# Kernel tuning notes

Measured on AMD Instinct MI355X. Metric: run time of the kernel, lower is better.

Reference implementation:

```python
import jax, jax.numpy as jnp
import numpy as np

B, C, O, K, H, W, CH = 32, 256, 256, 3, 56, 56, 4  # batch, in_planes, out_planes, kernel, spatial, in_chunk
STRIDE, PAD, DIL = 1, 1, 1


def setup_inputs() -> dict:
    key = jax.random.key(0)
    ks = jax.random.split(key, 5)
    gain = np.sqrt(2.0).astype(np.float32)  # calculate_gain('relu')
    x = jax.random.normal(ks[0], (B, C, H, W), jnp.float32)
    # CWFF: fc1 1x1 conv (C->C, no bias), fc2 1x1 conv (C->CH*C, bias)
    fc1_w = jax.random.normal(ks[1], (C, C), jnp.float32) * np.sqrt(2.0 / C).astype(np.float32)  # kaiming fan_out
    fc2_w = jax.random.normal(ks[2], (CH * C, C), jnp.float32) * np.sqrt(2.0 / (CH * C)).astype(np.float32)
    fc2_b = jnp.zeros((CH * C,), jnp.float32)
    cog_weight = jax.random.normal(ks[3], (O, CH, K, K), jnp.float32) * (gain * (CH * K * K) ** -0.5)
    weight = jax.random.normal(ks[4], (O, C, K, K), jnp.float32) * (gain * (C * K * K) ** -0.5)
    return dict(x=x, fc1_w=fc1_w, fc2_w=fc2_w, fc2_b=fc2_b, cog_weight=cog_weight, weight=weight)


def reference(x, fc1_w, fc2_w, fc2_b, cog_weight, weight):
    # CWFF: global avg pool -> 1x1 conv -> relu -> 1x1 conv
    pooled = x.mean(axis=(2, 3))                       # [B, C]
    h = jax.nn.relu(pooled @ fc1_w.T)                  # [B, C]
    kern = h @ fc2_w.T + fc2_b                         # [B, CH*C]
    # torch view(-1, in_chunk, 1, 1): channel dim splits as (c, ch)
    kern = kern.reshape(B, C, CH)                      # [B, C, CH]
    # cognitive weights: conv2d(cog_weight, kernel) == contraction over in_chunk
    cw = jnp.einsum('bct,otij->bocij', kern, cog_weight)   # [B, O, C, K, K]
    dyn_w = jax.nn.sigmoid(cw) * weight[None]               # per-sample kernels [B, O, C, K, K]
    # per-sample conv (groups=B in the original grouped-conv trick)
    def conv1(xi, wi):
        return jax.lax.conv_general_dilated(
            xi[None], wi,
            window_strides=(STRIDE, STRIDE),
            padding=[(PAD, PAD), (PAD, PAD)],
            rhs_dilation=(DIL, DIL))[0]
    return jax.vmap(conv1)(x, dyn_w)                   # [B, O, H, W]
```

## Files before the change

kernel.cpp:

```cpp
#include <hip/hip_runtime.h>

typedef unsigned short u16;
typedef __attribute__((ext_vector_type(4))) float f32x4;
typedef __attribute__((ext_vector_type(8))) short s16x8;
typedef __attribute__((ext_vector_type(4))) unsigned short u16x4;

static __device__ __forceinline__ u16 f2bf(float f) {
    unsigned int x = __float_as_uint(f);
    x += 0x7fffu + ((x >> 16) & 1u);
    return (u16)(x >> 16);
}

__global__ __launch_bounds__(256) void pool_kernel(const float* __restrict__ x,
                                                   float* __restrict__ pooled) {
    int bc = blockIdx.x;
    const float* p = x + (size_t)bc * 3136;
    float s = 0.f;
    for (int i = threadIdx.x; i < 784; i += 256) {
        f32x4 v = *(const f32x4*)(p + i * 4);
        s += v.x + v.y + v.z + v.w;
    }
#pragma unroll
    for (int off = 32; off; off >>= 1) s += __shfl_xor(s, off);
    __shared__ float red[4];
    int lane = threadIdx.x & 63, wave = threadIdx.x >> 6;
    if (lane == 0) red[wave] = s;
    __syncthreads();
    if (threadIdx.x == 0)
        pooled[bc] = (red[0] + red[1] + red[2] + red[3]) * (1.0f / 3136.0f);
}

__global__ __launch_bounds__(256) void fc1_kernel(const float* __restrict__ pooled,
                                                  const float* __restrict__ w,
                                                  float* __restrict__ h) {
    __shared__ float pv[256];
    int b = blockIdx.x >> 6;
    pv[threadIdx.x] = pooled[b * 256 + threadIdx.x];
    __syncthreads();
    int lane = threadIdx.x & 63, wave = threadIdx.x >> 6;
    int i = ((blockIdx.x & 63) << 2) + wave;
    f32x4 v = *(const f32x4*)(w + i * 256 + lane * 4);
    float s = v.x * pv[lane * 4 + 0] + v.y * pv[lane * 4 + 1] +
              v.z * pv[lane * 4 + 2] + v.w * pv[lane * 4 + 3];
#pragma unroll
    for (int off = 32; off; off >>= 1) s += __shfl_xor(s, off);
    if (lane == 0) h[b * 256 + i] = fmaxf(s, 0.f);
}

__global__ __launch_bounds__(256) void fc2_kernel(const float* __restrict__ h,
                                                  const float* __restrict__ w,
                                                  const float* __restrict__ bias,
                                                  float* __restrict__ kern) {
    __shared__ float hv[256];
    int b = blockIdx.x >> 8;
    hv[threadIdx.x] = h[b * 256 + threadIdx.x];
    __syncthreads();
    int lane = threadIdx.x & 63, wave = threadIdx.x >> 6;
    int i = ((blockIdx.x & 255) << 2) + wave;
    f32x4 v = *(const f32x4*)(w + i * 256 + lane * 4);
    float s = v.x * hv[lane * 4 + 0] + v.y * hv[lane * 4 + 1] +
              v.z * hv[lane * 4 + 2] + v.w * hv[lane * 4 + 3];
#pragma unroll
    for (int off = 32; off; off >>= 1) s += __shfl_xor(s, off);
    if (lane == 0) kern[b * 1024 + i] = s + bias[i];
}

__global__ __launch_bounds__(256) void dynw_kernel(const float* __restrict__ kern,
                                                   const float* __restrict__ cogw,
                                                   const float* __restrict__ wgt,
                                                   u16* __restrict__ dynw) {
    __shared__ float wl[2304];
    const int o = blockIdx.x & 255;
    const int bg = blockIdx.x >> 8;
    const int c = threadIdx.x;
    const float* wo = wgt + (size_t)o * 2304;
#pragma unroll
    for (int j = 0; j < 9; ++j)
        wl[j * 256 + c] = wo[j * 256 + c];
    __syncthreads();

    float cg0[9], cg1[9], cg2[9], cg3[9];
#pragma unroll
    for (int p = 0; p < 9; ++p) {
        cg0[p] = cogw[(o * 4 + 0) * 9 + p];
        cg1[p] = cogw[(o * 4 + 1) * 9 + p];
        cg2[p] = cogw[(o * 4 + 2) * 9 + p];
        cg3[p] = cogw[(o * 4 + 3) * 9 + p];
    }
    float w9[9];
#pragma unroll
    for (int p = 0; p < 9; ++p) w9[p] = wl[c * 9 + p];

    for (int b = bg * 8; b < bg * 8 + 8; ++b) {
        f32x4 k4 = *(const f32x4*)(kern + b * 1024 + c * 4);
        u16* dst = dynw + (size_t)(b * 256 + o) * 9 * 256 + c;
#pragma unroll
        for (int p = 0; p < 9; ++p) {
            float cw = k4.x * cg0[p] + k4.y * cg1[p] + k4.z * cg2[p] + k4.w * cg3[p];
            float sg = 1.0f / (1.0f + __expf(-cw));
            dst[p * 256] = f2bf(sg * w9[p]);
        }
    }
}

#define LDSW 40
__global__ __launch_bounds__(256, 2) void conv_kernel(const float* __restrict__ x,
                                                      const u16* __restrict__ dynw,
                                                      float* __restrict__ out) {
    __shared__ u16 lds[4 * 58 * LDSW];
    const int tid = threadIdx.x;
    const int wave = tid >> 6, lane = tid & 63;
    const int l15 = lane & 15, quad = lane >> 4;
    const int gid = blockIdx.x;
    const int slot = gid >> 3;
    const int b = (gid & 7) * 4 + slot / 28;
    const int stile = slot % 28;
    const int y0 = stile * 2;

    if (tid < 64) {
        int side = tid & 1, yy = (tid >> 1) & 3, cg = tid >> 3;
        *(u16x4*)&lds[(yy * 58 + (side ? 57 : 0)) * LDSW + cg * 4] = (u16x4){0, 0, 0, 0};
    }

    f32x4 acc[4][7];
#pragma unroll
    for (int mf = 0; mf < 4; ++mf)
#pragma unroll
        for (int nf = 0; nf < 7; ++nf) acc[mf][nf] = (f32x4){0.f, 0.f, 0.f, 0.f};

    int bbase[7];
#pragma unroll
    for (int nf = 0; nf < 7; ++nf) {
        int n = nf * 16 + l15;
        int r = (n >= 56) ? 1 : 0;
        int xx = n - 56 * r;
        bbase[nf] = (r * 58 + xx) * LDSW + quad * 8;
    }
    const u16* Abase = dynw + ((size_t)b * 256 + wave * 64 + l15) * 2304 + quad * 8;
    const float* Xb = x + (size_t)b * 256 * 3136;

    __syncthreads();
    for (int cc = 0; cc < 8; ++cc) {
#pragma unroll
        for (int it = 0; it < 7; ++it) {
            int i = it * 256 + tid;
            int q = i / 56;
            int xx = i - q * 56;
            int yy = q & 3;
            int cg = q >> 2;
            int yg = y0 - 1 + yy;
            u16x4 w = (u16x4){0, 0, 0, 0};
            if ((unsigned)yg < 56u) {
                const float* src = Xb + (size_t)(cc * 32 + cg * 4) * 3136 + yg * 56 + xx;
                w.x = f2bf(src[0]);
                w.y = f2bf(src[3136]);
                w.z = f2bf(src[2 * 3136]);
                w.w = f2bf(src[3 * 3136]);
            }
            *(u16x4*)&lds[(yy * 58 + 1 + xx) * LDSW + cg * 4] = w;
        }
        __syncthreads();
#pragma unroll
        for (int p = 0; p < 9; ++p) {
            const int dy = p / 3, dx = p % 3;
            const int tapoff = (dy * 58 + dx) * LDSW;
            s16x8 a0 = *(const s16x8*)(Abase + 0 * 36864 + p * 256 + cc * 32);
            s16x8 a1 = *(const s16x8*)(Abase + 1 * 36864 + p * 256 + cc * 32);
            s16x8 a2 = *(const s16x8*)(Abase + 2 * 36864 + p * 256 + cc * 32);
            s16x8 a3 = *(const s16x8*)(Abase + 3 * 36864 + p * 256 + cc * 32);
#pragma unroll
            for (int nf = 0; nf < 7; ++nf) {
                s16x8 bf = *(const s16x8*)(&lds[bbase[nf] + tapoff]);
                acc[0][nf] = __builtin_amdgcn_mfma_f32_16x16x32_bf16(a0, bf, acc[0][nf], 0, 0, 0);
                acc[1][nf] = __builtin_amdgcn_mfma_f32_16x16x32_bf16(a1, bf, acc[1][nf], 0, 0, 0);
                acc[2][nf] = __builtin_amdgcn_mfma_f32_16x16x32_bf16(a2, bf, acc[2][nf], 0, 0, 0);
                acc[3][nf] = __builtin_amdgcn_mfma_f32_16x16x32_bf16(a3, bf, acc[3][nf], 0, 0, 0);
            }
        }
        __syncthreads();
    }
#pragma unroll
    for (int mf = 0; mf < 4; ++mf) {
        int o = wave * 64 + mf * 16 + quad * 4;
        size_t obase = ((size_t)b * 256 + o) * 3136 + (size_t)stile * 112 + l15;
#pragma unroll
        for (int nf = 0; nf < 7; ++nf) {
#pragma unroll
            for (int r = 0; r < 4; ++r)
                out[obase + (size_t)r * 3136 + nf * 16] = acc[mf][nf][r];
        }
    }
}

extern "C" void kernel_launch(void* const* d_in, const int* in_sizes, int n_in,
                              void* d_out, int out_size, void* d_ws, size_t ws_size,
                              hipStream_t stream) {
    const float* x    = (const float*)d_in[0];
    const float* fc1w = (const float*)d_in[1];
    const float* fc2w = (const float*)d_in[2];
    const float* fc2b = (const float*)d_in[3];
    const float* cogw = (const float*)d_in[4];
    const float* wgt  = (const float*)d_in[5];
    float* out = (float*)d_out;

    char* ws = (char*)d_ws;
    float* pooled = (float*)ws;
    float* h      = (float*)(ws + 32768);
    float* kern   = (float*)(ws + 65536);
    u16*   dynw   = (u16*)(ws + 196608);

    pool_kernel<<<8192, 256, 0, stream>>>(x, pooled);
    fc1_kernel<<<2048, 256, 0, stream>>>(pooled, fc1w, h);
    fc2_kernel<<<8192, 256, 0, stream>>>(h, fc2w, fc2b, kern);
    dynw_kernel<<<1024, 256, 0, stream>>>(kern, cogw, wgt, dynw);
    conv_kernel<<<896, 256, 0, stream>>>(x, dynw, out);
}
```

Before: 384.6 us.

## Double-buffer conv input tiles in LDS with register prefetch of next chunk

The conv kernel now keeps two LDS buffers for the input halo tile. It issues global loads for the next 32-channel chunk into registers before running the MFMA loop on the current chunk, then converts those values to bf16 and writes them into the other buffer. This lets global-load latency overlap with matrix compute and removes one barrier per iteration. In exchange it uses 28 extra float registers plus precomputed offsets, which raises register pressure under the 2-blocks-per-SM launch bound, and it doubles LDS use.

```diff
diff --git a/kernel.cpp b/kernel.cpp
--- a/kernel.cpp
+++ b/kernel.cpp
@@ -107,7 +107,7 @@
 __global__ __launch_bounds__(256, 2) void conv_kernel(const float* __restrict__ x,
                                                       const u16* __restrict__ dynw,
                                                       float* __restrict__ out) {
-    __shared__ u16 lds[4 * 58 * LDSW];
+    __shared__ u16 lds[2][4 * 58 * LDSW];
     const int tid = threadIdx.x;
     const int wave = tid >> 6, lane = tid & 63;
     const int l15 = lane & 15, quad = lane >> 4;
@@ -117,9 +117,10 @@
     const int stile = slot % 28;
     const int y0 = stile * 2;
 
-    if (tid < 64) {
-        int side = tid & 1, yy = (tid >> 1) & 3, cg = tid >> 3;
-        *(u16x4*)&lds[(yy * 58 + (side ? 57 : 0)) * LDSW + cg * 4] = (u16x4){0, 0, 0, 0};
+    if (tid < 128) {
+        int cg = tid & 7, yy = (tid >> 3) & 3, side = (tid >> 5) & 1, bu = tid >> 6;
+        *(u16x4*)&lds[bu][(yy * 58 + (side ? 57 : 0)) * LDSW + cg * 4] =
+            (u16x4){0, 0, 0, 0};
     }
 
     f32x4 acc[4][7];
@@ -139,27 +140,44 @@
     const u16* Abase = dynw + ((size_t)b * 256 + wave * 64 + l15) * 2304 + quad * 8;
     const float* Xb = x + (size_t)b * 256 * 3136;
 
-    __syncthreads();
+    int st_goff[7], st_lds[7];
+    bool st_ok[7];
+#pragma unroll
+    for (int it = 0; it < 7; ++it) {
+        int i = it * 256 + tid;
+        int q = i / 56;
+        int xx = i - q * 56;
+        int yy = q & 3, cg = q >> 2;
+        int yg = y0 - 1 + yy;
+        st_ok[it] = (unsigned)yg < 56u;
+        st_goff[it] = cg * 4 * 3136 + (st_ok[it] ? yg * 56 + xx : 0);
+        st_lds[it] = (yy * 58 + 1 + xx) * LDSW + cg * 4;
+    }
+
+    float p0[7], p1[7], p2[7], p3[7];
+#define LOADC(cc)                                                         \
+    _Pragma("unroll") for (int it = 0; it < 7; ++it) {                    \
+        const float* s = Xb + (size_t)(cc) * 32 * 3136 + st_goff[it];     \
+        p0[it] = st_ok[it] ? s[0] : 0.f;                                  \
+        p1[it] = st_ok[it] ? s[3136] : 0.f;                               \
+        p2[it] = st_ok[it] ? s[2 * 3136] : 0.f;                           \
+        p3[it] = st_ok[it] ? s[3 * 3136] : 0.f;                           \
+    }
+#define WRITEC(bu)                                                        \
+    _Pragma("unroll") for (int it = 0; it < 7; ++it) {                    \
+        u16x4 w = (u16x4){f2bf(p0[it]), f2bf(p1[it]),                     \
+                          f2bf(p2[it]), f2bf(p3[it])};                    \
+        *(u16x4*)&lds[bu][st_lds[it]] = w;                                \
+    }
+
+    LOADC(0)
+    WRITEC(0)
+    __syncthreads();
+
     for (int cc = 0; cc < 8; ++cc) {
-#pragma unroll
-        for (int it = 0; it < 7; ++it) {
-            int i = it * 256 + tid;
-            int q = i / 56;
-            int xx = i - q * 56;
-            int yy = q & 3;
-            int cg = q >> 2;
-            int yg = y0 - 1 + yy;
-            u16x4 w = (u16x4){0, 0, 0, 0};
-            if ((unsigned)yg < 56u) {
-                const float* src = Xb + (size_t)(cc * 32 + cg * 4) * 3136 + yg * 56 + xx;
-                w.x = f2bf(src[0]);
-                w.y = f2bf(src[3136]);
-                w.z = f2bf(src[2 * 3136]);
-                w.w = f2bf(src[3 * 3136]);
-            }
-            *(u16x4*)&lds[(yy * 58 + 1 + xx) * LDSW + cg * 4] = w;
-        }
-        __syncthreads();
+        const int cur = cc & 1;
+        if (cc < 7) { LOADC(cc + 1) }
+        const u16* Lb = &lds[cur][0];
 #pragma unroll
         for (int p = 0; p < 9; ++p) {
             const int dy = p / 3, dx = p % 3;
@@ -170,15 +188,17 @@
             s16x8 a3 = *(const s16x8*)(Abase + 3 * 36864 + p * 256 + cc * 32);
 #pragma unroll
             for (int nf = 0; nf < 7; ++nf) {
-                s16x8 bf = *(const s16x8*)(&lds[bbase[nf] + tapoff]);
+                s16x8 bf = *(const s16x8*)(Lb + bbase[nf] + tapoff);
                 acc[0][nf] = __builtin_amdgcn_mfma_f32_16x16x32_bf16(a0, bf, acc[0][nf], 0, 0, 0);
                 acc[1][nf] = __builtin_amdgcn_mfma_f32_16x16x32_bf16(a1, bf, acc[1][nf], 0, 0, 0);
                 acc[2][nf] = __builtin_amdgcn_mfma_f32_16x16x32_bf16(a2, bf, acc[2][nf], 0, 0, 0);
                 acc[3][nf] = __builtin_amdgcn_mfma_f32_16x16x32_bf16(a3, bf, acc[3][nf], 0, 0, 0);
             }
         }
+        if (cc < 7) { WRITEC(1 - cur) }
         __syncthreads();
     }
+
 #pragma unroll
     for (int mf = 0; mf < 4; ++mf) {
         int o = wave * 64 + mf * 16 + quad * 4;
```

Result: slower. 399.1 us (+3.8%).

## Split conv output channels across two blocks and vectorize input staging loads

Applied to the files above, without the earlier changes.

The conv kernel now splits the 256 output channels into two halves handled by separate blocks, doubling the grid and halving per-wave accumulators so launch bounds allow four blocks per CU. The input tile staging now reads float4 along x for one channel instead of gathering four channels with scalar loads, then scatters bf16 values into LDS. The aim is higher occupancy and more coalesced global reads. In exchange, each input tile is loaded and converted twice, and the LDS stores become scalar 16-bit writes that may hit bank conflicts.

```diff
diff --git a/kernel.cpp b/kernel.cpp
--- a/kernel.cpp
+++ b/kernel.cpp
@@ -104,7 +104,7 @@
 }
 
 #define LDSW 40
-__global__ __launch_bounds__(256, 2) void conv_kernel(const float* __restrict__ x,
+__global__ __launch_bounds__(256, 4) void conv_kernel(const float* __restrict__ x,
                                                       const u16* __restrict__ dynw,
                                                       float* __restrict__ out) {
     __shared__ u16 lds[4 * 58 * LDSW];
@@ -113,8 +113,10 @@
     const int l15 = lane & 15, quad = lane >> 4;
     const int gid = blockIdx.x;
     const int slot = gid >> 3;
-    const int b = (gid & 7) * 4 + slot / 28;
-    const int stile = slot % 28;
+    const int b = (gid & 7) * 4 + slot / 56;
+    const int r2 = slot % 56;
+    const int stile = r2 >> 1;
+    const int ohalf = r2 & 1;
     const int y0 = stile * 2;
 
     if (tid < 64) {
@@ -122,9 +124,9 @@
         *(u16x4*)&lds[(yy * 58 + (side ? 57 : 0)) * LDSW + cg * 4] = (u16x4){0, 0, 0, 0};
     }
 
-    f32x4 acc[4][7];
-#pragma unroll
-    for (int mf = 0; mf < 4; ++mf)
+    f32x4 acc[2][7];
+#pragma unroll
+    for (int mf = 0; mf < 2; ++mf)
 #pragma unroll
         for (int nf = 0; nf < 7; ++nf) acc[mf][nf] = (f32x4){0.f, 0.f, 0.f, 0.f};
 
@@ -136,7 +138,8 @@
         int xx = n - 56 * r;
         bbase[nf] = (r * 58 + xx) * LDSW + quad * 8;
     }
-    const u16* Abase = dynw + ((size_t)b * 256 + wave * 64 + l15) * 2304 + quad * 8;
+    const u16* Abase = dynw +
+        ((size_t)b * 256 + ohalf * 128 + wave * 32 + l15) * 2304 + quad * 8;
     const float* Xb = x + (size_t)b * 256 * 3136;
 
     __syncthreads();
@@ -144,20 +147,17 @@
 #pragma unroll
         for (int it = 0; it < 7; ++it) {
             int i = it * 256 + tid;
-            int q = i / 56;
-            int xx = i - q * 56;
-            int yy = q & 3;
-            int cg = q >> 2;
+            int c = i / 56, rem = i % 56;
+            int yy = rem / 14, xg = rem % 14;
             int yg = y0 - 1 + yy;
-            u16x4 w = (u16x4){0, 0, 0, 0};
-            if ((unsigned)yg < 56u) {
-                const float* src = Xb + (size_t)(cc * 32 + cg * 4) * 3136 + yg * 56 + xx;
-                w.x = f2bf(src[0]);
-                w.y = f2bf(src[3136]);
-                w.z = f2bf(src[2 * 3136]);
-                w.w = f2bf(src[3 * 3136]);
-            }
-            *(u16x4*)&lds[(yy * 58 + 1 + xx) * LDSW + cg * 4] = w;
+            f32x4 v = (f32x4){0.f, 0.f, 0.f, 0.f};
+            if ((unsigned)yg < 56u)
+                v = *(const f32x4*)(Xb + (size_t)(cc * 32 + c) * 3136 + yg * 56 + xg * 4);
+            int base = (yy * 58 + 1 + xg * 4) * LDSW + c;
+            lds[base]            = f2bf(v.x);
+            lds[base + LDSW]     = f2bf(v.y);
+            lds[base + 2 * LDSW] = f2bf(v.z);
+            lds[base + 3 * LDSW] = f2bf(v.w);
         }
         __syncthreads();
 #pragma unroll
@@ -166,22 +166,18 @@
             const int tapoff = (dy * 58 + dx) * LDSW;
             s16x8 a0 = *(const s16x8*)(Abase + 0 * 36864 + p * 256 + cc * 32);
             s16x8 a1 = *(const s16x8*)(Abase + 1 * 36864 + p * 256 + cc * 32);
-            s16x8 a2 = *(const s16x8*)(Abase + 2 * 36864 + p * 256 + cc * 32);
-            s16x8 a3 = *(const s16x8*)(Abase + 3 * 36864 + p * 256 + cc * 32);
 #pragma unroll
             for (int nf = 0; nf < 7; ++nf) {
                 s16x8 bf = *(const s16x8*)(&lds[bbase[nf] + tapoff]);
                 acc[0][nf] = __builtin_amdgcn_mfma_f32_16x16x32_bf16(a0, bf, acc[0][nf], 0, 0, 0);
                 acc[1][nf] = __builtin_amdgcn_mfma_f32_16x16x32_bf16(a1, bf, acc[1][nf], 0, 0, 0);
-                acc[2][nf] = __builtin_amdgcn_mfma_f32_16x16x32_bf16(a2, bf, acc[2][nf], 0, 0, 0);
-                acc[3][nf] = __builtin_amdgcn_mfma_f32_16x16x32_bf16(a3, bf, acc[3][nf], 0, 0, 0);
             }
         }
         __syncthreads();
     }
 #pragma unroll
-    for (int mf = 0; mf < 4; ++mf) {
-        int o = wave * 64 + mf * 16 + quad * 4;
+    for (int mf = 0; mf < 2; ++mf) {
+        int o = ohalf * 128 + wave * 32 + mf * 16 + quad * 4;
         size_t obase = ((size_t)b * 256 + o) * 3136 + (size_t)stile * 112 + l15;
 #pragma unroll
         for (int nf = 0; nf < 7; ++nf) {
@@ -213,5 +209,5 @@
     fc1_kernel<<<2048, 256, 0, stream>>>(pooled, fc1w, h);
     fc2_kernel<<<8192, 256, 0, stream>>>(h, fc2w, fc2b, kern);
     dynw_kernel<<<1024, 256, 0, stream>>>(kern, cogw, wgt, dynw);
-    conv_kernel<<<896, 256, 0, stream>>>(x, dynw, out);
-}
+    conv_kernel<<<1792, 256, 0, stream>>>(x, dynw, out);
+}
```

Measured after the change: 391.4 us. Within noise of the previous version (+1.8%).
